# Kernel tuning notes

Hardware: AMD Instinct MI355X
Metric: run time of the kernel (lower is better)

Reference implementation:

```python
import jax, jax.numpy as jnp
import numpy as np

LATENT = 128
LN_EPS = 1e-3  # keras LayerNormalization default epsilon


def _mlp(x, W0, b0, W1, b1, W2, b2, gamma, beta):
    # two relu hidden layers + linear output + layer norm (MeshGraphNets style)
    h = jax.nn.relu(x @ W0 + b0)
    h = jax.nn.relu(h @ W1 + b1)
    h = h @ W2 + b2
    mu = jnp.mean(h, axis=-1, keepdims=True)
    var = jnp.var(h, axis=-1, keepdims=True)
    return (h - mu) * jax.lax.rsqrt(var + LN_EPS) * gamma + beta


def setup_inputs() -> dict:
    key = jax.random.key(0)
    ks = jax.random.split(key, 12)
    N, D, E = 10000, 128, 320000
    cat = 3 * D  # sender + receiver + edge features concatenated
    s = lambda fan: 1.0 / np.sqrt(fan)
    return {
        "sender_features": jax.random.normal(ks[0], (N, D), jnp.float32),
        "receiver_features": jax.random.normal(ks[1], (N, D), jnp.float32),
        "edge_features": jax.random.normal(ks[2], (E, D), jnp.float32),
        "senders": jax.random.randint(ks[3], (E,), 0, N, jnp.int32),
        "receivers": jax.random.randint(ks[4], (E,), 0, N, jnp.int32),
        "W0": jax.random.normal(ks[5], (cat, LATENT), jnp.float32) * s(cat),
        "b0": jnp.zeros((LATENT,), jnp.float32),
        "W1": jax.random.normal(ks[6], (LATENT, LATENT), jnp.float32) * s(LATENT),
        "b1": jnp.zeros((LATENT,), jnp.float32),
        "W2": jax.random.normal(ks[7], (LATENT, LATENT), jnp.float32) * s(LATENT),
        "b2": jnp.zeros((LATENT,), jnp.float32),
        "gamma": jnp.ones((LATENT,), jnp.float32),
        "beta": jnp.zeros((LATENT,), jnp.float32),
    }


def reference(sender_features, receiver_features, edge_features, senders,
              receivers, W0, b0, W1, b1, W2, b2, gamma, beta):
    g_send = jnp.take(sender_features, senders, axis=0)      # [E, D]
    g_recv = jnp.take(receiver_features, receivers, axis=0)  # [E, D]
    feats = jnp.concatenate([g_send, g_recv, edge_features], axis=-1)  # [E, 3D]
    return _mlp(feats, W0, b0, W1, b1, W2, b2, gamma, beta)  # [E, LATENT]
```

## Files before the change

kernel.cpp:

```cpp
#include <hip/hip_runtime.h>
#include <stdint.h>


typedef __attribute__((ext_vector_type(8)))  short    s16x8;
typedef __attribute__((ext_vector_type(8)))  _Float16 f16x8;
typedef __attribute__((ext_vector_type(16))) float    f32x16;
typedef __attribute__((ext_vector_type(4)))  float    f32x4;

__device__ __forceinline__ f32x16 mfma16(f16x8 a, f16x8 b, f32x16 c) {
  return __builtin_amdgcn_mfma_f32_32x32x16_f16(a, b, c, 0, 0, 0);
}

__global__ void prep_weights(const float* __restrict__ W0,
                             const float* __restrict__ W1,
                             const float* __restrict__ W2,
                             short* __restrict__ ws) {
  int tid = blockIdx.x * 256 + threadIdx.x;
  const float* W;
  int rel, imgbase, perm;
  if (tid < 6144)      { W = W0; rel = tid;        imgbase = 0;     perm = 0; }
  else if (tid < 8192) { W = W1; rel = tid - 6144; imgbase = 49152; perm = 1; }
  else                 { W = W2; rel = tid - 8192; imgbase = 65536; perm = 1; }
  int n     = rel & 127;
  int chunk = rel >> 7;
  int slab  = chunk >> 3;
  int kc    = chunk & 7;
  s16x8 o;
#pragma unroll
  for (int j = 0; j < 8; ++j) {
    int kslot = slab * 64 + kc * 8 + j;
    int ktrue = perm ? ((kslot & ~12) | ((kslot & 4) << 1) | ((kslot & 8) >> 1))
                     : kslot;
    float v = W[(size_t)ktrue * 128 + n];
    o[j] = __builtin_bit_cast(short, (_Float16)v);
  }
  *(s16x8*)(ws + imgbase + slab * 8192 + n * 64 + ((kc ^ (n & 7)) << 3)) = o;
}

__device__ __forceinline__ void stage(const short* __restrict__ ws, int s,
                                      char* lds, int tid) {
  char* buf = lds + (s & 3) * 16384;
  const char* g = (const char*)ws + s * 16384;
#pragma unroll
  for (int i = 0; i < 2; ++i) {
    char* lp = buf + (i * 512 + (tid & ~63)) * 16;
    const char* gp = g + (i * 512 + tid) * 16;
    __builtin_amdgcn_global_load_lds(
        (__attribute__((address_space(1))) const void*)gp,
        (__attribute__((address_space(3))) void*)lp, 16, 0, 0);
  }
}

__device__ __forceinline__ void kstep(const char* buf, int q, int lg1,
                                      int e31, f16x8 xf, f32x16* acc) {
  const int kc = q * 2 + lg1;
  const int slot = (kc ^ (e31 & 7)) << 4;
#pragma unroll
  for (int nt = 0; nt < 4; ++nt) {
    int n = nt * 32 + e31;
    s16x8 wf = *(const s16x8*)(buf + n * 128 + slot);
    acc[nt] = mfma16(__builtin_bit_cast(f16x8, wf), xf, acc[nt]);
  }
}

__device__ __forceinline__ void transition(const float* __restrict__ b,
                                           int lg1, f32x16* acc, f16x8* fr) {
#pragma unroll
  for (int ks = 0; ks < 8; ++ks) {
    const int nt = ks >> 1;
#pragma unroll
    for (int jq = 0; jq < 2; ++jq) {
      int nb = nt * 32 + 16 * (ks & 1) + 8 * jq + 4 * lg1;
      f32x4 bv = *(const f32x4*)(b + nb);
#pragma unroll
      for (int r = 0; r < 4; ++r) {
        float h = acc[nt][8 * (ks & 1) + jq * 4 + r] + bv[r];
        fr[ks][jq * 4 + r] = (_Float16)fmaxf(h, 0.0f);
      }
    }
  }
}

__device__ __forceinline__ void zero_acc(f32x16* acc) {
#pragma unroll
  for (int nt = 0; nt < 4; ++nt)
#pragma unroll
    for (int i = 0; i < 16; ++i) acc[nt][i] = 0.0f;
}

__global__ __launch_bounds__(512, 4) void edge_mlp(
    const float* __restrict__ sf, const float* __restrict__ rf,
    const float* __restrict__ ef, const int* __restrict__ snd,
    const int* __restrict__ rcv, const short* __restrict__ wt,
    const float* __restrict__ b0, const float* __restrict__ b1,
    const float* __restrict__ b2, const float* __restrict__ gamma,
    const float* __restrict__ beta, float* __restrict__ out) {
  __shared__ __align__(16) char lds[65536];
  const int tid = threadIdx.x;
  const int w   = tid >> 6;
  const int lane = tid & 63;
  const int e31 = lane & 31;
  const int lg1 = lane >> 5;
  const int e   = blockIdx.x * 256 + w * 32 + e31;
  const int sidx = snd[e];
  const int ridx = rcv[e];

  const float* xbase0 = sf + (size_t)sidx * 128 + lg1 * 8;
  const float* xbase1 = rf + (size_t)ridx * 128 + lg1 * 8;
  const float* xbase2 = ef + (size_t)e    * 128 + lg1 * 8;

#define XPTR(t) ((t) < 8 ? xbase0 + (t) * 16 \
                : (t) < 16 ? xbase1 + ((t) - 8) * 16 \
                : xbase2 + ((t) - 16) * 16)

  f32x16 acc[4];
  zero_acc(acc);
  f32x4 xa[24], xb[24];

  stage(wt, 0, lds, tid);
  stage(wt, 1, lds, tid);
  { const float* p0 = XPTR(0); xa[0] = *(const f32x4*)p0; xb[0] = *(const f32x4*)(p0 + 4);
    const float* p1 = XPTR(1); xa[1] = *(const f32x4*)p1; xb[1] = *(const f32x4*)(p1 + 4); }
  __syncthreads();

#pragma unroll
  for (int s = 0; s < 6; ++s) {
    stage(wt, s + 2, lds, tid);
    const char* buf = lds + (s & 3) * 16384;
#pragma unroll
    for (int q = 0; q < 4; ++q) {
      const int t = s * 4 + q;
      if (t + 2 < 24) {
        const float* p = XPTR(t + 2);
        xa[t + 2] = *(const f32x4*)p;
        xb[t + 2] = *(const f32x4*)(p + 4);
      }
      f16x8 xf;
#pragma unroll
      for (int j = 0; j < 4; ++j) {
        xf[j]     = (_Float16)xa[t][j];
        xf[4 + j] = (_Float16)xb[t][j];
      }
      kstep(buf, q, lg1, e31, xf, acc);
    }
    __syncthreads();
  }

  f16x8 fr[8];
  transition(b0, lg1, acc, fr);
  zero_acc(acc);

#pragma unroll
  for (int s = 6; s < 8; ++s) {
    stage(wt, s + 2, lds, tid);
    const char* buf = lds + (s & 3) * 16384;
#pragma unroll
    for (int q = 0; q < 4; ++q) kstep(buf, q, lg1, e31, fr[(s - 6) * 4 + q], acc);
    __syncthreads();
  }

  transition(b1, lg1, acc, fr);
  zero_acc(acc);

#pragma unroll
  for (int s = 8; s < 10; ++s) {
    const char* buf = lds + (s & 3) * 16384;
#pragma unroll
    for (int q = 0; q < 4; ++q) kstep(buf, q, lg1, e31, fr[(s - 8) * 4 + q], acc);
  }

  float sum = 0.0f, sq = 0.0f;
#pragma unroll
  for (int nt = 0; nt < 4; ++nt)
#pragma unroll
    for (int qq = 0; qq < 4; ++qq) {
      int nb = nt * 32 + qq * 8 + 4 * lg1;
      f32x4 bv = *(const f32x4*)(b2 + nb);
#pragma unroll
      for (int r = 0; r < 4; ++r) {
        float v = acc[nt][qq * 4 + r] + bv[r];
        acc[nt][qq * 4 + r] = v;
        sum += v;
        sq  += v * v;
      }
    }
  sum += __shfl_xor(sum, 32, 64);
  sq  += __shfl_xor(sq, 32, 64);
  const float mu  = sum * (1.0f / 128.0f);
  const float var = sq * (1.0f / 128.0f) - mu * mu;
  const float rs  = rsqrtf(var + 1e-3f);

  float* op = out + (size_t)e * 128;
#pragma unroll
  for (int nt = 0; nt < 4; ++nt)
#pragma unroll
    for (int qq = 0; qq < 4; ++qq) {
      int nb = nt * 32 + qq * 8 + 4 * lg1;
      f32x4 g  = *(const f32x4*)(gamma + nb);
      f32x4 bt = *(const f32x4*)(beta + nb);
      f32x4 o;
#pragma unroll
      for (int r = 0; r < 4; ++r)
        o[r] = (acc[nt][qq * 4 + r] - mu) * rs * g[r] + bt[r];
      *(f32x4*)(op + nb) = o;
    }
#undef XPTR
}

extern "C" void kernel_launch(void* const* d_in, const int* in_sizes, int n_in,
                              void* d_out, int out_size, void* d_ws, size_t ws_size,
                              hipStream_t stream) {
  const float* sf    = (const float*)d_in[0];
  const float* rf    = (const float*)d_in[1];
  const float* ef    = (const float*)d_in[2];
  const int*   snd   = (const int*)d_in[3];
  const int*   rcv   = (const int*)d_in[4];
  const float* W0    = (const float*)d_in[5];
  const float* b0    = (const float*)d_in[6];
  const float* W1    = (const float*)d_in[7];
  const float* b1    = (const float*)d_in[8];
  const float* W2    = (const float*)d_in[9];
  const float* b2    = (const float*)d_in[10];
  const float* gamma = (const float*)d_in[11];
  const float* beta  = (const float*)d_in[12];
  short* wt = (short*)d_ws;

  prep_weights<<<40, 256, 0, stream>>>(W0, W1, W2, wt);
  edge_mlp<<<1250, 512, 0, stream>>>(sf, rf, ef, snd, rcv, wt,
                                     b0, b1, b2, gamma, beta, (float*)d_out);
}
```

Baseline: 426.2 us.

## Hand-schedule edge MLP pipeline with triple-buffered weights and explicit vmcnt waits

Replaces the looped 4-slot weight staging with a fully unrolled 3-slot LDS ring. Explicit s_waitcnt vmcnt counts and raw barriers replace __syncthreads, so global loads stay in flight across barriers. The input prefetch window shrinks from 24 registers to 5, cutting register pressure. Biases, gamma and beta are loaded once into LDS, and the output is transposed through LDS so each lane writes contiguous row segments. The hand-counted vmcnt values are fragile: a miscount or a compiler reordering of loads could cause races or stalls.

```diff
diff --git a/kernel.cpp b/kernel.cpp
--- a/kernel.cpp
+++ b/kernel.cpp
@@ -6,6 +6,10 @@
 typedef __attribute__((ext_vector_type(8)))  _Float16 f16x8;
 typedef __attribute__((ext_vector_type(16))) float    f32x16;
 typedef __attribute__((ext_vector_type(4)))  float    f32x4;
+
+#define FENCE asm volatile("" ::: "memory")
+#define VMWAIT(N) asm volatile("s_waitcnt vmcnt(" #N ")" ::: "memory")
+#define BARRIER do { __builtin_amdgcn_s_barrier(); asm volatile("" ::: "memory"); } while (0)
 
 __device__ __forceinline__ f32x16 mfma16(f16x8 a, f16x8 b, f32x16 c) {
   return __builtin_amdgcn_mfma_f32_32x32x16_f16(a, b, c, 0, 0, 0);
@@ -38,8 +42,8 @@
 }
 
 __device__ __forceinline__ void stage(const short* __restrict__ ws, int s,
-                                      char* lds, int tid) {
-  char* buf = lds + (s & 3) * 16384;
+                                      int slot, char* lds, int tid) {
+  char* buf = lds + slot * 16384;
   const char* g = (const char*)ws + s * 16384;
 #pragma unroll
   for (int i = 0; i < 2; ++i) {
@@ -95,116 +99,183 @@
     const float* __restrict__ b0, const float* __restrict__ b1,
     const float* __restrict__ b2, const float* __restrict__ gamma,
     const float* __restrict__ beta, float* __restrict__ out) {
-  __shared__ __align__(16) char lds[65536];
-  const int tid = threadIdx.x;
-  const int w   = tid >> 6;
+  __shared__ __align__(16) char lds[52224];
+  const int tid  = threadIdx.x;
+  const int w    = tid >> 6;
   const int lane = tid & 63;
-  const int e31 = lane & 31;
-  const int lg1 = lane >> 5;
-  const int e   = blockIdx.x * 256 + w * 32 + e31;
+  const int e31  = lane & 31;
+  const int lg1  = lane >> 5;
+  const int eb   = blockIdx.x * 256 + w * 32;
+  const int e    = eb + e31;
+
+  if (w < 3) {
+    const float* s0 = (w == 0) ? b0 : (w == 1) ? b2 : beta;
+    const float* s1 = (w == 0) ? b1 : (w == 1) ? gamma : beta;
+    const float* src = ((lane < 32) ? s0 : s1) + (lane & 31) * 4;
+    char* dst = lds + 49152 + w * 1024;
+    __builtin_amdgcn_global_load_lds(
+        (__attribute__((address_space(1))) const void*)src,
+        (__attribute__((address_space(3))) void*)dst, 16, 0, 0);
+  }
+  FENCE;
   const int sidx = snd[e];
   const int ridx = rcv[e];
+  FENCE;
+  stage(wt, 0, 0, lds, tid);
+  FENCE;
+  stage(wt, 1, 1, lds, tid);
+  FENCE;
 
   const float* xbase0 = sf + (size_t)sidx * 128 + lg1 * 8;
   const float* xbase1 = rf + (size_t)ridx * 128 + lg1 * 8;
   const float* xbase2 = ef + (size_t)e    * 128 + lg1 * 8;
-
 #define XPTR(t) ((t) < 8 ? xbase0 + (t) * 16 \
                 : (t) < 16 ? xbase1 + ((t) - 8) * 16 \
                 : xbase2 + ((t) - 16) * 16)
+#define XISSUE(t) do { const float* p_ = XPTR(t); \
+    xa[(t) % 5] = *(const f32x4*)p_; xb[(t) % 5] = *(const f32x4*)(p_ + 4); } while (0)
+#define KSTEP0(t, buf) do { \
+    f16x8 xf_; f32x4 A_ = xa[(t) % 5], B_ = xb[(t) % 5]; \
+    xf_[0]=(_Float16)A_[0]; xf_[1]=(_Float16)A_[1]; xf_[2]=(_Float16)A_[2]; xf_[3]=(_Float16)A_[3]; \
+    xf_[4]=(_Float16)B_[0]; xf_[5]=(_Float16)B_[1]; xf_[6]=(_Float16)B_[2]; xf_[7]=(_Float16)B_[3]; \
+    kstep((buf), (t) & 3, lg1, e31, xf_, acc); } while (0)
 
   f32x16 acc[4];
   zero_acc(acc);
-  f32x4 xa[24], xb[24];
-
-  stage(wt, 0, lds, tid);
-  stage(wt, 1, lds, tid);
-  { const float* p0 = XPTR(0); xa[0] = *(const f32x4*)p0; xb[0] = *(const f32x4*)(p0 + 4);
-    const float* p1 = XPTR(1); xa[1] = *(const f32x4*)p1; xb[1] = *(const f32x4*)(p1 + 4); }
-  __syncthreads();
-
-#pragma unroll
-  for (int s = 0; s < 6; ++s) {
-    stage(wt, s + 2, lds, tid);
-    const char* buf = lds + (s & 3) * 16384;
-#pragma unroll
-    for (int q = 0; q < 4; ++q) {
-      const int t = s * 4 + q;
-      if (t + 2 < 24) {
-        const float* p = XPTR(t + 2);
-        xa[t + 2] = *(const f32x4*)p;
-        xb[t + 2] = *(const f32x4*)(p + 4);
-      }
-      f16x8 xf;
-#pragma unroll
-      for (int j = 0; j < 4; ++j) {
-        xf[j]     = (_Float16)xa[t][j];
-        xf[4 + j] = (_Float16)xb[t][j];
-      }
-      kstep(buf, q, lg1, e31, xf, acc);
-    }
-    __syncthreads();
-  }
+  f32x4 xa[5], xb[5];
+  XISSUE(0); XISSUE(1); XISSUE(2); XISSUE(3); XISSUE(4);
+  FENCE;
+  VMWAIT(12); BARRIER;
 
   f16x8 fr[8];
-  transition(b0, lg1, acc, fr);
-  zero_acc(acc);
-
-#pragma unroll
-  for (int s = 6; s < 8; ++s) {
-    stage(wt, s + 2, lds, tid);
-    const char* buf = lds + (s & 3) * 16384;
-#pragma unroll
-    for (int q = 0; q < 4; ++q) kstep(buf, q, lg1, e31, fr[(s - 6) * 4 + q], acc);
-    __syncthreads();
-  }
-
-  transition(b1, lg1, acc, fr);
-  zero_acc(acc);
-
-#pragma unroll
-  for (int s = 8; s < 10; ++s) {
-    const char* buf = lds + (s & 3) * 16384;
-#pragma unroll
-    for (int q = 0; q < 4; ++q) kstep(buf, q, lg1, e31, fr[(s - 8) * 4 + q], acc);
-  }
-
-  float sum = 0.0f, sq = 0.0f;
+
+  { const char* buf = lds;
+    stage(wt, 2, 2, lds, tid);
+    KSTEP0(0, buf); XISSUE(5);
+    KSTEP0(1, buf); XISSUE(6);
+    KSTEP0(2, buf); XISSUE(7);
+    KSTEP0(3, buf); XISSUE(8);
+    VMWAIT(20); BARRIER; }
+  { const char* buf = lds + 16384;
+    stage(wt, 3, 0, lds, tid);
+    KSTEP0(4, buf); XISSUE(9);
+    KSTEP0(5, buf); XISSUE(10);
+    KSTEP0(6, buf); XISSUE(11);
+    KSTEP0(7, buf); XISSUE(12);
+    VMWAIT(18); BARRIER; }
+  { const char* buf = lds + 32768;
+    stage(wt, 4, 1, lds, tid);
+    KSTEP0(8, buf); XISSUE(13);
+    KSTEP0(9, buf); XISSUE(14);
+    KSTEP0(10, buf); XISSUE(15);
+    KSTEP0(11, buf); XISSUE(16);
+    VMWAIT(18); BARRIER; }
+  { const char* buf = lds;
+    stage(wt, 5, 2, lds, tid);
+    KSTEP0(12, buf); XISSUE(17);
+    KSTEP0(13, buf); XISSUE(18);
+    KSTEP0(14, buf); XISSUE(19);
+    KSTEP0(15, buf); XISSUE(20);
+    VMWAIT(18); BARRIER; }
+  { const char* buf = lds + 16384;
+    stage(wt, 6, 0, lds, tid);
+    KSTEP0(16, buf); XISSUE(21);
+    KSTEP0(17, buf); XISSUE(22);
+    KSTEP0(18, buf); XISSUE(23);
+    KSTEP0(19, buf);
+    VMWAIT(16); BARRIER; }
+  { const char* buf = lds + 32768;
+    stage(wt, 7, 1, lds, tid);
+    KSTEP0(20, buf);
+    KSTEP0(21, buf);
+    KSTEP0(22, buf);
+    KSTEP0(23, buf);
+    transition((const float*)(lds + 49152), lg1, acc, fr);
+    zero_acc(acc);
+    VMWAIT(8); BARRIER; }
+
+  { const char* buf = lds;
+    stage(wt, 8, 2, lds, tid);
+    kstep(buf, 0, lg1, e31, fr[0], acc);
+    kstep(buf, 1, lg1, e31, fr[1], acc);
+    kstep(buf, 2, lg1, e31, fr[2], acc);
+    kstep(buf, 3, lg1, e31, fr[3], acc);
+    VMWAIT(2); BARRIER; }
+  { const char* buf = lds + 16384;
+    stage(wt, 9, 0, lds, tid);
+    kstep(buf, 0, lg1, e31, fr[4], acc);
+    kstep(buf, 1, lg1, e31, fr[5], acc);
+    kstep(buf, 2, lg1, e31, fr[6], acc);
+    kstep(buf, 3, lg1, e31, fr[7], acc);
+    transition((const float*)(lds + 49152 + 512), lg1, acc, fr);
+    zero_acc(acc);
+    VMWAIT(2); BARRIER; }
+
+  { const char* buf = lds + 32768;
+    kstep(buf, 0, lg1, e31, fr[0], acc);
+    kstep(buf, 1, lg1, e31, fr[1], acc);
+    kstep(buf, 2, lg1, e31, fr[2], acc);
+    kstep(buf, 3, lg1, e31, fr[3], acc);
+    VMWAIT(0); BARRIER; }
+  { const char* buf = lds;
+    kstep(buf, 0, lg1, e31, fr[4], acc);
+    kstep(buf, 1, lg1, e31, fr[5], acc);
+    kstep(buf, 2, lg1, e31, fr[6], acc);
+    kstep(buf, 3, lg1, e31, fr[7], acc);
+  }
+  BARRIER;
+
+  const float* pb2 = (const float*)(lds + 49152 + 1024);
+  const float* pg  = (const float*)(lds + 49152 + 1536);
+  const float* pbt = (const float*)(lds + 49152 + 2048);
+  float sum = 0.f, sq = 0.f;
 #pragma unroll
   for (int nt = 0; nt < 4; ++nt)
 #pragma unroll
     for (int qq = 0; qq < 4; ++qq) {
-      int nb = nt * 32 + qq * 8 + 4 * lg1;
-      f32x4 bv = *(const f32x4*)(b2 + nb);
+      f32x4 bv = *(const f32x4*)(pb2 + nt * 32 + qq * 8 + 4 * lg1);
 #pragma unroll
       for (int r = 0; r < 4; ++r) {
         float v = acc[nt][qq * 4 + r] + bv[r];
         acc[nt][qq * 4 + r] = v;
-        sum += v;
-        sq  += v * v;
+        sum += v; sq += v * v;
       }
     }
   sum += __shfl_xor(sum, 32, 64);
   sq  += __shfl_xor(sq, 32, 64);
-  const float mu  = sum * (1.0f / 128.0f);
-  const float var = sq * (1.0f / 128.0f) - mu * mu;
-  const float rs  = rsqrtf(var + 1e-3f);
-
-  float* op = out + (size_t)e * 128;
-#pragma unroll
-  for (int nt = 0; nt < 4; ++nt)
+  const float mu = sum * (1.0f / 128.0f);
+  const float rs = rsqrtf(sq * (1.0f / 128.0f) - mu * mu + 1e-3f);
+
+  float* T = (float*)lds + w * 1056;
+  const int l4 = lane >> 2, ch = lane & 3;
+#pragma unroll
+  for (int p = 0; p < 4; ++p) {
 #pragma unroll
     for (int qq = 0; qq < 4; ++qq) {
-      int nb = nt * 32 + qq * 8 + 4 * lg1;
-      f32x4 g  = *(const f32x4*)(gamma + nb);
-      f32x4 bt = *(const f32x4*)(beta + nb);
-      f32x4 o;
+      const int n0 = p * 32 + qq * 8 + 4 * lg1;
+      f32x4 g4 = *(const f32x4*)(pg + n0);
+      f32x4 t4 = *(const f32x4*)(pbt + n0);
 #pragma unroll
       for (int r = 0; r < 4; ++r)
-        o[r] = (acc[nt][qq * 4 + r] - mu) * rs * g[r] + bt[r];
-      *(f32x4*)(op + nb) = o;
+        T[e31 * 33 + qq * 8 + 4 * lg1 + r] =
+            (acc[p][qq * 4 + r] - mu) * rs * g4[r] + t4[r];
     }
+#pragma unroll
+    for (int bb = 0; bb < 2; ++bb) {
+      const int el = bb * 16 + l4;
+      float* orow = out + (size_t)(eb + el) * 128 + p * 32 + ch * 4;
+#pragma unroll
+      for (int j = 0; j < 2; ++j) {
+        f32x4 ov;
+#pragma unroll
+        for (int k = 0; k < 4; ++k) ov[k] = T[el * 33 + j * 16 + ch * 4 + k];
+        *(f32x4*)(orow + j * 16) = ov;
+      }
+    }
+  }
 #undef XPTR
+#undef XISSUE
+#undef KSTEP0
 }
 
 extern "C" void kernel_launch(void* const* d_in, const int* in_sizes, int n_in,
```

New measurement: 441.3 us. +3.6%, slower.
